# Performance work log

Measured on AMD Instinct MI355X. Metric: run time of the kernel, lower is better.

The kernel has to match this reference:

```python
import jax, jax.numpy as jnp
import numpy as np

# Static dims
N = 512        # nodes
T = 8          # window_size
E = 16384      # edges per timestep
F0, H1, FP = 128, 256, 64   # feat_proj_dims
FN = 16        # noise dim
WIN = FP + FN  # WLE in_channels = 80
WH = 128       # WLE hidden
D_SSM = 1      # TLSSM d_model = d_ssm = 1 (scalar per node pair)
D_STATE = 16
D_CONV = 4
CONV_DIM = D_SSM + 2 * D_STATE          # 33
D_IN = 2 * D_SSM + 2 * D_STATE + 1      # z, xBC, dt -> 35
PRED = 1


def setup_inputs() -> dict:
    key = jax.random.key(0)
    ks = jax.random.split(key, 24)
    s = 0.05
    rn = lambda k, shp: jax.random.normal(k, shp, dtype=jnp.float32) * s
    return {
        "edge_index": jax.random.randint(ks[0], (T, 2, E), 0, N, dtype=jnp.int64),
        "edge_weight": jax.random.uniform(ks[1], (T, E), dtype=jnp.float32),
        "feats": jax.random.normal(ks[2], (T, N, F0), dtype=jnp.float32),
        "noise": jax.random.normal(ks[3], (T, N, FN), dtype=jnp.float32),
        # feat_proj MLP
        "Wp1": rn(ks[4], (F0, H1)), "bp1": jnp.zeros((H1,), jnp.float32),
        "Wp2": rn(ks[5], (H1, FP)), "bp2": jnp.zeros((FP,), jnp.float32),
        # WeightedLinkEncoder
        "wle_W1": rn(ks[6], (WIN, WH)), "wle_b1": jnp.zeros((WH,), jnp.float32),
        "wle_W2": rn(ks[7], (WH, WH)), "wle_b2": jnp.zeros((WH,), jnp.float32),
        "wle_W3": rn(ks[8], (WH, WH)), "wle_b3": jnp.zeros((WH,), jnp.float32),
        "wle_w4": rn(ks[9], (WH, 1)), "wle_b4": jnp.zeros((1,), jnp.float32),
        # TLSSM (Mamba2-style stepwise)
        "W_in": rn(ks[10], (D_SSM, D_IN)),
        "conv_w": rn(ks[11], (CONV_DIM, D_CONV)),
        "conv_b": jnp.zeros((CONV_DIM,), jnp.float32),
        "dt_bias": jnp.zeros((1,), jnp.float32),
        "A_log": jnp.zeros((1,), jnp.float32),
        "D_skip": jnp.ones((1,), jnp.float32) * s,
        "W_out": rn(ks[12], (D_SSM, D_SSM)),
    }


def _forward(edge_index, edge_weight, feats, noise,
             Wp1, bp1, Wp2, bp2,
             wle_W1, wle_b1, wle_W2, wle_b2, wle_W3, wle_b3, wle_w4, wle_b4,
             W_in, conv_w, conv_b, dt_bias, A_log, D_skip, W_out):
    # feat_proj: stacked Linear+ReLU, vectorized over timesteps
    h = jax.nn.relu(feats @ Wp1 + bp1)
    h = jax.nn.relu(h @ Wp2 + bp2)              # [T, N, FP]
    emb = jnp.concatenate([h, noise], axis=-1)

    # WeightedLinkEncoder: node MLP -> weighted sparse propagation -> edge score
    def wle(x, ei, ew):
        hh = jax.nn.relu(x @ wle_W1 + wle_b1)                       # [N, WH]
        msg = ew[:, None] * hh[ei[1]]                               # gather neighbors
        agg = jax.ops.segment_sum(msg, ei[0], num_segments=N)      # scatter-add
        h2 = jax.nn.relu((hh + agg) @ wle_W2 + wle_b2)
        ef = h2[ei[0]] * h2[ei[1]]                                 # per-edge hadamard
        s = jax.nn.relu(ef @ wle_W3 + wle_b3) @ wle_w4 + wle_b4    # [E, 1]
        return s[:, 0]

    scores = jax.vmap(wle)(emb, edge_index, edge_weight)            # [T, E]

    # SparseTensor(...).to_dense(): densify edge scores to N x N per step
    def dens(ei, s):
        return jnp.zeros((N, N), scores.dtype).at[ei[0], ei[1]].set(s)

    dense = jax.vmap(dens)(edge_index, scores).reshape(T, N * N, D_SSM)

    # TLSSM stepwise recurrence over the window, batch = N*N
    A = -jnp.exp(A_log)  # [1]

    def step(carry, xt):
        conv_state, ssm_state = carry                    # [BN,CONV_DIM,D_CONV], [BN,D_SSM,D_STATE]
        zxbcdt = xt @ W_in                               # [BN, D_IN]
        z, xBC, dt = jnp.split(zxbcdt, [D_SSM, D_SSM + CONV_DIM], axis=-1)
        conv_state = jnp.concatenate([conv_state[:, :, 1:], xBC[:, :, None]], axis=-1)
        xBC = jax.nn.silu(jnp.sum(conv_state * conv_w, axis=-1) + conv_b)
        x_, Bm, Cm = jnp.split(xBC, [D_SSM, D_SSM + D_STATE], axis=-1)
        dt = jax.nn.softplus(dt + dt_bias)               # [BN, 1]
        dA = jnp.exp(dt * A)                             # [BN, 1]
        ssm_state = ssm_state * dA[:, :, None] + (dt * x_)[:, :, None] * Bm[:, None, :]
        y = jnp.sum(ssm_state * Cm[:, None, :], axis=-1) + D_skip * x_
        y = y * jax.nn.silu(z)
        return (conv_state, ssm_state), y @ W_out

    conv0 = jnp.zeros((N * N, CONV_DIM, D_CONV), jnp.float32)
    ssm0 = jnp.zeros((N * N, D_SSM, D_STATE), jnp.float32)
    _, ys = jax.lax.scan(step, (conv0, ssm0), dense)     # [T, BN, 1]
    out = ys.reshape(T, N, N)[-PRED:]                    # pred_flag=True: last pred_size steps
    return out


def reference(edge_index, edge_weight, feats, noise,
              Wp1, bp1, Wp2, bp2,
              wle_W1, wle_b1, wle_W2, wle_b2, wle_W3, wle_b3, wle_w4, wle_b4,
              W_in, conv_w, conv_b, dt_bias, A_log, D_skip, W_out):
    return _forward(edge_index, edge_weight, feats, noise,
                    Wp1, bp1, Wp2, bp2,
                    wle_W1, wle_b1, wle_W2, wle_b2, wle_W3, wle_b3, wle_w4, wle_b4,
                    W_in, conv_w, conv_b, dt_bias, A_log, D_skip, W_out)
```

## Files before the change

kernel.cpp:

```cpp
#include <hip/hip_runtime.h>
#include <math.h>

#define Nn 512
#define Tt 8
#define Ee 16384
#define NNc (Nn*Nn)
#define TNr (Tt*Nn)
#define TE  (Tt*Ee)
#define CAP 128

typedef __bf16 bf16x8 __attribute__((ext_vector_type(8)));
typedef float  f32x4  __attribute__((ext_vector_type(4)));
union BU { uint4 q; bf16x8 v; };

__device__ __forceinline__ void dec2(float x0, float x1, unsigned &hi, unsigned &lo){
    unsigned u0 = __float_as_uint(x0), u1 = __float_as_uint(x1);
    unsigned t0 = u0 + 0x7FFFu + ((u0>>16)&1u);
    unsigned t1 = u1 + 0x7FFFu + ((u1>>16)&1u);
    hi = (t0>>16) | (t1 & 0xFFFF0000u);
    float h0 = __uint_as_float(t0 & 0xFFFF0000u);
    float h1 = __uint_as_float(t1 & 0xFFFF0000u);
    float l0 = x0 - h0, l1 = x1 - h1;
    unsigned v0 = __float_as_uint(l0), v1 = __float_as_uint(l1);
    unsigned s0 = v0 + 0x7FFFu + ((v0>>16)&1u);
    unsigned s1 = v1 + 0x7FFFu + ((v1>>16)&1u);
    lo = (s0>>16) | (s1 & 0xFFFF0000u);
}

__global__ __launch_bounds__(256) void k_pf(
    const int* __restrict__ ei, const float* __restrict__ W3,
    unsigned short* __restrict__ w3h, unsigned short* __restrict__ w3l,
    int* __restrict__ cnt, int* __restrict__ tag, float4* __restrict__ out4,
    const float* __restrict__ feats, const float* __restrict__ noise,
    const float* __restrict__ Wp1, const float* __restrict__ bp1,
    const float* __restrict__ Wp2, const float* __restrict__ bp2,
    const float* __restrict__ W1, const float* __restrict__ b1,
    float* __restrict__ hh)
{
    __shared__ float sfeat[16][128];
    __shared__ float sh1[16][256];
    __shared__ float semb[16][80];
    int tid = threadIdx.x;
    if (blockIdx.x < 64){
        int e = blockIdx.x*256 + tid;
        int a = ei[7*2*Ee + e], b = ei[7*2*Ee + Ee + e];
        int cell = a*Nn + b;
#pragma unroll
        for (int t=0;t<8;++t) tag[t*NNc + cell] = 0;
        if (e < TNr) cnt[e] = 0;
        float4 z = {0.f,0.f,0.f,0.f};
#pragma unroll
        for (int q=0;q<4;++q) out4[q*16384 + e] = z;
        int i    = e & 7;
        int lane = (e>>3) & 63;
        int jt   = (e>>9) & 7;
        int kt   = e>>12;
        int k = kt*32 + (lane>>4)*8 + i;
        int j = jt*16 + (lane&15);
        float x = W3[k*128 + j];
        unsigned u = __float_as_uint(x);
        unsigned t = u + 0x7FFFu + ((u>>16)&1u);
        w3h[e] = (unsigned short)(t>>16);
        float hf = __uint_as_float(t & 0xFFFF0000u);
        float lf = x - hf;
        unsigned v = __float_as_uint(lf);
        unsigned s = v + 0x7FFFu + ((v>>16)&1u);
        w3l[e] = (unsigned short)(s>>16);
        return;
    }
    int r0 = (blockIdx.x - 64) * 16;
#pragma unroll
    for (int k = 0; k < 8; ++k) {
        int lin = k*256 + tid;
        sfeat[lin>>7][lin&127] = feats[(size_t)r0*128 + lin];
    }
    {
        int r = tid>>4, k = tid&15;
        semb[r][64+k] = noise[(size_t)(r0+r)*16 + k];
    }
    __syncthreads();
    {
        int j = tid;
        float acc[16];
#pragma unroll
        for (int r=0;r<16;++r) acc[r]=0.f;
        for (int i=0;i<128;i+=4) {
            float w0=Wp1[(i+0)*256+j], w1=Wp1[(i+1)*256+j];
            float w2=Wp1[(i+2)*256+j], w3=Wp1[(i+3)*256+j];
#pragma unroll
            for (int r=0;r<16;++r) {
                float4 f = *(const float4*)&sfeat[r][i];
                acc[r] += f.x*w0 + f.y*w1 + f.z*w2 + f.w*w3;
            }
        }
        float b = bp1[j];
#pragma unroll
        for (int r=0;r<16;++r) sh1[r][j] = fmaxf(acc[r]+b, 0.f);
    }
    __syncthreads();
    {
        int jo = tid & 63;
        int rr = tid >> 6;
        float b2v = bp2[jo];
        for (int rg=0; rg<4; ++rg) {
            int r = rg*4 + rr;
            float a2 = 0.f;
            for (int i=0;i<256;i+=4) {
                float4 f = *(const float4*)&sh1[r][i];
                a2 += f.x*Wp2[(i+0)*64+jo] + f.y*Wp2[(i+1)*64+jo]
                    + f.z*Wp2[(i+2)*64+jo] + f.w*Wp2[(i+3)*64+jo];
            }
            semb[r][jo] = fmaxf(a2+b2v, 0.f);
        }
    }
    __syncthreads();
    {
        int j = tid & 127;
        int rb = (tid>>7)*8;
        float acc[8];
#pragma unroll
        for (int r=0;r<8;++r) acc[r]=0.f;
        for (int i=0;i<80;i+=4) {
            float w0=W1[(i+0)*128+j], w1=W1[(i+1)*128+j];
            float w2=W1[(i+2)*128+j], w3=W1[(i+3)*128+j];
#pragma unroll
            for (int r=0;r<8;++r) {
                float4 f = *(const float4*)&semb[rb+r][i];
                acc[r] += f.x*w0 + f.y*w1 + f.z*w2 + f.w*w3;
            }
        }
        float b = b1[j];
#pragma unroll
        for (int r=0;r<8;++r) hh[(size_t)(r0+rb+r)*128 + j] = fmaxf(acc[r]+b, 0.f);
    }
}

__global__ __launch_bounds__(256) void k_histtag(
    const int* __restrict__ ei, const float* __restrict__ ew,
    int* __restrict__ cnt, int2* __restrict__ bucket2, int* __restrict__ tag)
{
    int g = blockIdx.x*256 + threadIdx.x;
    int t = g>>14, e = g&(Ee-1);
    int a = ei[t*2*Ee + e];
    int b = ei[t*2*Ee + Ee + e];
    int cell = t*Nn + a;
    int pos = atomicAdd(&cnt[cell], 1);
    if (pos < CAP) bucket2[(size_t)cell*CAP + pos] = make_int2(b, __float_as_int(ew[g]));
    atomicMax(&tag[t*NNc + a*Nn + b], g+1);
}

__global__ __launch_bounds__(256) void k_sw(
    const float* __restrict__ hh, const int* __restrict__ cnt,
    const int2* __restrict__ bucket2,
    const float* __restrict__ W2, const float* __restrict__ b2,
    float* __restrict__ h2)
{
    __shared__ float sx[2][128];
    int dloc = threadIdx.x >> 7;
    int ch = threadIdx.x & 127;
    int bidd = blockIdx.x*2 + dloc;
    int t = bidd >> 9;
    int n = cnt[bidd]; n = n < CAP ? n : CAP;
    const int2* __restrict__ bk = &bucket2[(size_t)bidd*CAP];
    const float* __restrict__ hht = &hh[(size_t)t*Nn*128];
    float acc = hh[(size_t)bidd*128 + ch];
    int i = 0;
    for (; i+1 < n; i += 2){
        int2 p0 = bk[i], p1 = bk[i+1];
        acc += __int_as_float(p0.y)*hht[(size_t)p0.x*128 + ch]
             + __int_as_float(p1.y)*hht[(size_t)p1.x*128 + ch];
    }
    if (i < n){
        int2 p = bk[i];
        acc += __int_as_float(p.y)*hht[(size_t)p.x*128 + ch];
    }
    sx[dloc][ch] = acc;
    __syncthreads();
    float s = 0.f;
    for (int i2=0; i2<128; i2+=4){
        float4 x = *(const float4*)&sx[dloc][i2];
        s += x.x*W2[(i2+0)*128+ch] + x.y*W2[(i2+1)*128+ch]
           + x.z*W2[(i2+2)*128+ch] + x.w*W2[(i2+3)*128+ch];
    }
    h2[(size_t)bidd*128 + ch] = fmaxf(s + b2[ch], 0.f);
}

__global__ __launch_bounds__(512) void k_edge9(
    const int* __restrict__ ei, const float* __restrict__ h2,
    const uint4* __restrict__ w3h, const uint4* __restrict__ w3l,
    const float* __restrict__ b3, const float* __restrict__ w4,
    const float* __restrict__ b4, float* __restrict__ sc)
{
    __shared__ uint4 sBh[2048];
    __shared__ uint4 sBl[2048];
    int tid = threadIdx.x;
    int bid = blockIdx.x;
#pragma unroll
    for (int q=0;q<4;++q){
        sBh[q*512+tid] = w3h[q*512+tid];
        sBl[q*512+tid] = w3l[q*512+tid];
    }
    int tb  = bid >> 6;
    int e0b = (bid & 63) * 256;
    int w   = tid >> 6, lane = tid & 63;
    int e0w = e0b + w*32;
    int r16 = lane & 15, g4 = lane >> 4;

    const int* __restrict__ eit = &ei[tb*2*Ee];
    int a0 = eit[e0w + r16],      s0 = eit[Ee + e0w + r16];
    int a1 = eit[e0w + 16 + r16], s1 = eit[Ee + e0w + 16 + r16];
    const float* __restrict__ pa0 = &h2[(size_t)(tb*Nn+a0)*128];
    const float* __restrict__ pb0 = &h2[(size_t)(tb*Nn+s0)*128];
    const float* __restrict__ pa1 = &h2[(size_t)(tb*Nn+a1)*128];
    const float* __restrict__ pb1 = &h2[(size_t)(tb*Nn+s1)*128];

    f32x4 acc0[8], acc1[8];
#pragma unroll
    for (int jt=0;jt<8;++jt){
        acc0[jt] = (f32x4){0.f,0.f,0.f,0.f};
        acc1[jt] = (f32x4){0.f,0.f,0.f,0.f};
    }

    float4 rA0,rA1,rB0,rB1,rC0,rC1,rD0,rD1;
#define LOADK(kt) { int k0=(kt)*32+g4*8; \
    rA0=*(const float4*)&pa0[k0]; rA1=*(const float4*)&pa0[k0+4]; \
    rB0=*(const float4*)&pb0[k0]; rB1=*(const float4*)&pb0[k0+4]; \
    rC0=*(const float4*)&pa1[k0]; rC1=*(const float4*)&pa1[k0+4]; \
    rD0=*(const float4*)&pb1[k0]; rD1=*(const float4*)&pb1[k0+4]; }

    BU ah0[2], al0[2], ah1[2], al1[2];
#define DECK(s) { uint4 hq,lq; \
    dec2(rA0.x*rB0.x, rA0.y*rB0.y, hq.x, lq.x); \
    dec2(rA0.z*rB0.z, rA0.w*rB0.w, hq.y, lq.y); \
    dec2(rA1.x*rB1.x, rA1.y*rB1.y, hq.z, lq.z); \
    dec2(rA1.z*rB1.z, rA1.w*rB1.w, hq.w, lq.w); \
    ah0[s].q=hq; al0[s].q=lq; \
    dec2(rC0.x*rD0.x, rC0.y*rD0.y, hq.x, lq.x); \
    dec2(rC0.z*rD0.z, rC0.w*rD0.w, hq.y, lq.y); \
    dec2(rC1.x*rD1.x, rC1.y*rD1.y, hq.z, lq.z); \
    dec2(rC1.z*rD1.z, rC1.w*rD1.w, hq.w, lq.w); \
    ah1[s].q=hq; al1[s].q=lq; }

    LOADK(0)
    DECK(0)
    __syncthreads();
#pragma unroll
    for (int kt=0;kt<4;++kt){
        if (kt < 3) LOADK(kt+1)
        const int s = kt & 1;
#pragma unroll
        for (int jt=0;jt<8;++jt){
            BU Bh, Bl;
            Bh.q = sBh[(kt*8+jt)*64 + lane];
            Bl.q = sBl[(kt*8+jt)*64 + lane];
            acc0[jt] = __builtin_amdgcn_mfma_f32_16x16x32_bf16(ah0[s].v, Bh.v, acc0[jt], 0,0,0);
            acc0[jt] = __builtin_amdgcn_mfma_f32_16x16x32_bf16(ah0[s].v, Bl.v, acc0[jt], 0,0,0);
            acc0[jt] = __builtin_amdgcn_mfma_f32_16x16x32_bf16(al0[s].v, Bh.v, acc0[jt], 0,0,0);
            acc1[jt] = __builtin_amdgcn_mfma_f32_16x16x32_bf16(ah1[s].v, Bh.v, acc1[jt], 0,0,0);
            acc1[jt] = __builtin_amdgcn_mfma_f32_16x16x32_bf16(ah1[s].v, Bl.v, acc1[jt], 0,0,0);
            acc1[jt] = __builtin_amdgcn_mfma_f32_16x16x32_bf16(al1[s].v, Bh.v, acc1[jt], 0,0,0);
        }
        if (kt < 3) DECK((kt+1)&1)
    }

    float b4v = b4[0];
    float b3v[8], w4v[8];
#pragma unroll
    for (int jt=0;jt<8;++jt){ b3v[jt] = b3[jt*16 + r16]; w4v[jt] = w4[jt*16 + r16]; }
#pragma unroll
    for (int r=0;r<4;++r){
        float p0 = 0.f, p1 = 0.f;
#pragma unroll
        for (int jt=0;jt<8;++jt){
            p0 += fmaxf(acc0[jt][r] + b3v[jt], 0.f) * w4v[jt];
            p1 += fmaxf(acc1[jt][r] + b3v[jt], 0.f) * w4v[jt];
        }
        p0 += __shfl_xor(p0,1); p0 += __shfl_xor(p0,2);
        p0 += __shfl_xor(p0,4); p0 += __shfl_xor(p0,8);
        p1 += __shfl_xor(p1,1); p1 += __shfl_xor(p1,2);
        p1 += __shfl_xor(p1,4); p1 += __shfl_xor(p1,8);
        if (r16 == 0){
            sc[(size_t)tb*Ee + e0w + g4*4 + r]      = p0 + b4v;
            sc[(size_t)tb*Ee + e0w + 16 + g4*4 + r] = p1 + b4v;
        }
    }
}

__global__ __launch_bounds__(256) void k_ssm2(
    const int* __restrict__ ei, const int* __restrict__ tag,
    const float* __restrict__ sc,
    const float* __restrict__ W_in, const float* __restrict__ conv_w,
    const float* __restrict__ conv_b, const float* __restrict__ dt_bias,
    const float* __restrict__ A_log, const float* __restrict__ D_skip,
    const float* __restrict__ W_out, float* __restrict__ out)
{
    __shared__ float scw[132], scb[33], swin[35];
    int tid = threadIdx.x;
    if (tid < 132) scw[tid] = conv_w[tid];
    if (tid < 33)  scb[tid] = conv_b[tid];
    if (tid < 35)  swin[tid] = W_in[tid];
    __syncthreads();

    int e = blockIdx.x*256 + tid;
    int a = ei[7*2*Ee + e], b = ei[7*2*Ee + Ee + e];
    int cell = a*Nn + b;
    float x[8];
#pragma unroll
    for (int t=0;t<8;++t){
        int tg = tag[t*NNc + cell];
        x[t] = (tg > 0) ? sc[tg-1] : 0.f;
    }

    float A    = -expf(A_log[0]);
    float dtb  = dt_bias[0];
    float dsk  = D_skip[0];
    float wout = W_out[0];
    float win_z = swin[0], win_dt = swin[34];

    float ssm[16];
#pragma unroll
    for (int q=0;q<16;++q) ssm[q]=0.f;
    float h0=0.f,h1=0.f,h2v=0.f;
    float y=0.f;
    for (int t=0;t<8;++t){
        float xt = x[t];
        float act[33];
#pragma unroll
        for (int c=0;c<33;++c){
            float s = h0*scw[c*4+0] + h1*scw[c*4+1] + h2v*scw[c*4+2] + xt*scw[c*4+3];
            float pre = swin[1+c]*s + scb[c];
            act[c] = pre / (1.f + expf(-pre));
        }
        float x_ = act[0];
        float dtr = xt*win_dt + dtb;
        float dt  = (dtr > 20.f) ? dtr : log1pf(expf(dtr));
        float dA  = expf(dt*A);
        float dx  = dt*x_;
        float yv = 0.f;
#pragma unroll
        for (int q=0;q<16;++q){
            ssm[q] = ssm[q]*dA + dx*act[1+q];
            yv += ssm[q]*act[17+q];
        }
        yv += dsk*x_;
        float z = xt*win_z;
        yv *= z / (1.f + expf(-z));
        y = yv;
        h0=h1; h1=h2v; h2v=xt;
    }
    out[cell] = y*wout;
}

extern "C" void kernel_launch(void* const* d_in, const int* in_sizes, int n_in,
                              void* d_out, int out_size, void* d_ws, size_t ws_size,
                              hipStream_t stream)
{
    const int*   ei    = (const int*)d_in[0];
    const float* ew    = (const float*)d_in[1];
    const float* feats = (const float*)d_in[2];
    const float* noise = (const float*)d_in[3];
    const float* Wp1=(const float*)d_in[4];  const float* bp1=(const float*)d_in[5];
    const float* Wp2=(const float*)d_in[6];  const float* bp2=(const float*)d_in[7];
    const float* W1 =(const float*)d_in[8];  const float* b1 =(const float*)d_in[9];
    const float* W2 =(const float*)d_in[10]; const float* b2 =(const float*)d_in[11];
    const float* W3 =(const float*)d_in[12]; const float* b3 =(const float*)d_in[13];
    const float* w4 =(const float*)d_in[14]; const float* b4 =(const float*)d_in[15];
    const float* W_in  =(const float*)d_in[16]; const float* conv_w=(const float*)d_in[17];
    const float* conv_b=(const float*)d_in[18]; const float* dt_bias=(const float*)d_in[19];
    const float* A_log =(const float*)d_in[20]; const float* D_skip=(const float*)d_in[21];
    const float* W_out =(const float*)d_in[22];

    float* out = (float*)d_out;
    float* ws  = (float*)d_ws;
    float* hh    = ws;
    float* h2    = hh    + 524288;
    float* sc    = h2    + 524288;
    int*   cnt   = (int*)(sc + 131072);
    int*   tag   = cnt + TNr;
    int2*  bucket2 = (int2*)(tag + 2097152);
    unsigned short* w3h = (unsigned short*)(bucket2 + (size_t)TNr*CAP);
    unsigned short* w3l = w3h + 16384;

    k_pf      <<<320, 256, 0, stream>>>(ei, W3, w3h, w3l, cnt, tag, (float4*)out,
                                        feats, noise, Wp1, bp1, Wp2, bp2, W1, b1, hh);
    k_histtag <<<TE/256, 256, 0, stream>>>(ei, ew, cnt, bucket2, tag);
    k_sw      <<<TNr/2, 256, 0, stream>>>(hh, cnt, bucket2, W2, b2, h2);
    k_edge9   <<<512, 512, 0, stream>>>(ei, h2, (const uint4*)w3h, (const uint4*)w3l,
                                        b3, w4, b4, sc);
    k_ssm2    <<<Ee/256, 256, 0, stream>>>(ei, tag, sc, W_in, conv_w, conv_b,
                                           dt_bias, A_log, D_skip, W_out, out);
}
```

Before: 107.2 us.

## Make feature-projection MLP wave-private to replace block barriers with wave barriers

The per-row feature projection MLP (two Linear+ReLU layers plus the first link-encoder layer) is reorganised so each 64-lane wave owns four rows end to end. That lets the block-wide __syncthreads be replaced by wave barriers. Weight loads are widened to float4/float2 so each lane computes several output columns. The likely cost is that Wp1, Wp2 and W1 are now fetched once per wave rather than once per block, raising global/L2 weight traffic. Register use per lane also changes.

```diff
diff --git a/kernel.cpp b/kernel.cpp
--- a/kernel.cpp
+++ b/kernel.cpp
@@ -68,70 +68,96 @@
         w3l[e] = (unsigned short)(s>>16);
         return;
     }
-    int r0 = (blockIdx.x - 64) * 16;
-#pragma unroll
-    for (int k = 0; k < 8; ++k) {
-        int lin = k*256 + tid;
-        sfeat[lin>>7][lin&127] = feats[(size_t)r0*128 + lin];
-    }
+    int w = tid >> 6, lane = tid & 63;
+    int lr = w*4;
+    int r0 = (blockIdx.x - 64)*16 + lr;
     {
-        int r = tid>>4, k = tid&15;
-        semb[r][64+k] = noise[(size_t)(r0+r)*16 + k];
-    }
-    __syncthreads();
+        const float4* __restrict__ src = (const float4*)&feats[(size_t)r0*128];
+        float4 v0 = src[lane], v1 = src[64+lane];
+        ((float4*)&sfeat[lr][0])[lane]    = v0;
+        ((float4*)&sfeat[lr][0])[64+lane] = v1;
+    }
     {
-        int j = tid;
-        float acc[16];
-#pragma unroll
-        for (int r=0;r<16;++r) acc[r]=0.f;
-        for (int i=0;i<128;i+=4) {
-            float w0=Wp1[(i+0)*256+j], w1=Wp1[(i+1)*256+j];
-            float w2=Wp1[(i+2)*256+j], w3=Wp1[(i+3)*256+j];
-#pragma unroll
-            for (int r=0;r<16;++r) {
-                float4 f = *(const float4*)&sfeat[r][i];
-                acc[r] += f.x*w0 + f.y*w1 + f.z*w2 + f.w*w3;
+        int r = lane >> 4, k = lane & 15;
+        semb[lr+r][64+k] = noise[(size_t)(r0+r)*16 + k];
+    }
+    __builtin_amdgcn_wave_barrier();
+    {
+        int jb = lane*4;
+        float acc[4][4];
+#pragma unroll
+        for (int r=0;r<4;++r)
+#pragma unroll
+            for (int q=0;q<4;++q) acc[r][q]=0.f;
+        for (int i=0;i<128;i+=4){
+            float4 w0 = *(const float4*)&Wp1[(i+0)*256 + jb];
+            float4 w1 = *(const float4*)&Wp1[(i+1)*256 + jb];
+            float4 w2 = *(const float4*)&Wp1[(i+2)*256 + jb];
+            float4 w3 = *(const float4*)&Wp1[(i+3)*256 + jb];
+#pragma unroll
+            for (int r=0;r<4;++r){
+                float4 f = *(const float4*)&sfeat[lr+r][i];
+                acc[r][0] += f.x*w0.x + f.y*w1.x + f.z*w2.x + f.w*w3.x;
+                acc[r][1] += f.x*w0.y + f.y*w1.y + f.z*w2.y + f.w*w3.y;
+                acc[r][2] += f.x*w0.z + f.y*w1.z + f.z*w2.z + f.w*w3.z;
+                acc[r][3] += f.x*w0.w + f.y*w1.w + f.z*w2.w + f.w*w3.w;
             }
         }
-        float b = bp1[j];
-#pragma unroll
-        for (int r=0;r<16;++r) sh1[r][j] = fmaxf(acc[r]+b, 0.f);
-    }
-    __syncthreads();
+        float4 b = *(const float4*)&bp1[jb];
+#pragma unroll
+        for (int r=0;r<4;++r){
+            float4 o;
+            o.x = fmaxf(acc[r][0]+b.x, 0.f);
+            o.y = fmaxf(acc[r][1]+b.y, 0.f);
+            o.z = fmaxf(acc[r][2]+b.z, 0.f);
+            o.w = fmaxf(acc[r][3]+b.w, 0.f);
+            *(float4*)&sh1[lr+r][jb] = o;
+        }
+    }
+    __builtin_amdgcn_wave_barrier();
     {
-        int jo = tid & 63;
-        int rr = tid >> 6;
-        float b2v = bp2[jo];
-        for (int rg=0; rg<4; ++rg) {
-            int r = rg*4 + rr;
-            float a2 = 0.f;
-            for (int i=0;i<256;i+=4) {
-                float4 f = *(const float4*)&sh1[r][i];
-                a2 += f.x*Wp2[(i+0)*64+jo] + f.y*Wp2[(i+1)*64+jo]
-                    + f.z*Wp2[(i+2)*64+jo] + f.w*Wp2[(i+3)*64+jo];
+        float a2[4] = {0.f,0.f,0.f,0.f};
+        for (int i=0;i<256;i+=4){
+            float w0 = Wp2[(i+0)*64 + lane];
+            float w1 = Wp2[(i+1)*64 + lane];
+            float w2 = Wp2[(i+2)*64 + lane];
+            float w3 = Wp2[(i+3)*64 + lane];
+#pragma unroll
+            for (int r=0;r<4;++r){
+                float4 f = *(const float4*)&sh1[lr+r][i];
+                a2[r] += f.x*w0 + f.y*w1 + f.z*w2 + f.w*w3;
             }
-            semb[r][jo] = fmaxf(a2+b2v, 0.f);
-        }
-    }
-    __syncthreads();
+        }
+        float b = bp2[lane];
+#pragma unroll
+        for (int r=0;r<4;++r) semb[lr+r][lane] = fmaxf(a2[r]+b, 0.f);
+    }
+    __builtin_amdgcn_wave_barrier();
     {
-        int j = tid & 127;
-        int rb = (tid>>7)*8;
-        float acc[8];
-#pragma unroll
-        for (int r=0;r<8;++r) acc[r]=0.f;
-        for (int i=0;i<80;i+=4) {
-            float w0=W1[(i+0)*128+j], w1=W1[(i+1)*128+j];
-            float w2=W1[(i+2)*128+j], w3=W1[(i+3)*128+j];
-#pragma unroll
-            for (int r=0;r<8;++r) {
-                float4 f = *(const float4*)&semb[rb+r][i];
-                acc[r] += f.x*w0 + f.y*w1 + f.z*w2 + f.w*w3;
+        int j2 = lane*2;
+        float a3[4][2];
+#pragma unroll
+        for (int r=0;r<4;++r){ a3[r][0]=0.f; a3[r][1]=0.f; }
+        for (int i=0;i<80;i+=4){
+            float2 w0 = *(const float2*)&W1[(i+0)*128 + j2];
+            float2 w1 = *(const float2*)&W1[(i+1)*128 + j2];
+            float2 w2 = *(const float2*)&W1[(i+2)*128 + j2];
+            float2 w3 = *(const float2*)&W1[(i+3)*128 + j2];
+#pragma unroll
+            for (int r=0;r<4;++r){
+                float4 f = *(const float4*)&semb[lr+r][i];
+                a3[r][0] += f.x*w0.x + f.y*w1.x + f.z*w2.x + f.w*w3.x;
+                a3[r][1] += f.x*w0.y + f.y*w1.y + f.z*w2.y + f.w*w3.y;
             }
         }
-        float b = b1[j];
-#pragma unroll
-        for (int r=0;r<8;++r) hh[(size_t)(r0+rb+r)*128 + j] = fmaxf(acc[r]+b, 0.f);
+        float2 bb = *(const float2*)&b1[j2];
+#pragma unroll
+        for (int r=0;r<4;++r){
+            float2 o;
+            o.x = fmaxf(a3[r][0]+bb.x, 0.f);
+            o.y = fmaxf(a3[r][1]+bb.y, 0.f);
+            *(float2*)&hh[(size_t)(r0+r)*128 + j2] = o;
+        }
     }
 }
 
```

Result: slower. 111.4 us (+3.9%).

## Move feature-projection MLP to split-bf16 MFMA and fuse it with edge histogram

Applied to the files above, without the earlier changes.

The three dense layers (feat_proj two layers plus the first WLE layer) move from scalar FP32 FMA loops to MFMA 16x16x32 bf16. A three-product hi/lo split keeps accuracy close to FP32. A new prep kernel pre-splits and swizzles Wp1, Wp2 and W1 into bf16 hi/lo tiles. The MLP blocks and the edge histogram/tag atomics now run in one launch, removing a kernel boundary and letting the two workloads overlap. The cost is an extra weight-conversion pass on every call and more scratch space, and the reduced-precision split may change the output slightly.

```diff
diff --git a/kernel.cpp b/kernel.cpp
--- a/kernel.cpp
+++ b/kernel.cpp
@@ -27,22 +27,38 @@
     lo = (s0>>16) | (s1 & 0xFFFF0000u);
 }
 
-__global__ __launch_bounds__(256) void k_pf(
+__device__ __forceinline__ void splitw(float x, unsigned short* ph, unsigned short* pl, int idx){
+    unsigned u = __float_as_uint(x);
+    unsigned t = u + 0x7FFFu + ((u>>16)&1u);
+    ph[idx] = (unsigned short)(t>>16);
+    float hf = __uint_as_float(t & 0xFFFF0000u);
+    float lf = x - hf;
+    unsigned v = __float_as_uint(lf);
+    unsigned s = v + 0x7FFFu + ((v>>16)&1u);
+    pl[idx] = (unsigned short)(s>>16);
+}
+
+#define DECA(Ah, Al, xa, ya) { uint4 hq, lq; \
+    dec2(xa.x, xa.y, hq.x, lq.x); \
+    dec2(xa.z, xa.w, hq.y, lq.y); \
+    dec2(ya.x, ya.y, hq.z, lq.z); \
+    dec2(ya.z, ya.w, hq.w, lq.w); \
+    Ah.q = hq; Al.q = lq; }
+
+__global__ __launch_bounds__(256) void k_prep(
     const int* __restrict__ ei, const float* __restrict__ W3,
+    const float* __restrict__ Wp1, const float* __restrict__ Wp2,
+    const float* __restrict__ W1,
     unsigned short* __restrict__ w3h, unsigned short* __restrict__ w3l,
-    int* __restrict__ cnt, int* __restrict__ tag, float4* __restrict__ out4,
-    const float* __restrict__ feats, const float* __restrict__ noise,
-    const float* __restrict__ Wp1, const float* __restrict__ bp1,
-    const float* __restrict__ Wp2, const float* __restrict__ bp2,
-    const float* __restrict__ W1, const float* __restrict__ b1,
-    float* __restrict__ hh)
-{
-    __shared__ float sfeat[16][128];
-    __shared__ float sh1[16][256];
-    __shared__ float semb[16][80];
+    unsigned short* __restrict__ p1h, unsigned short* __restrict__ p1l,
+    unsigned short* __restrict__ p2h, unsigned short* __restrict__ p2l,
+    unsigned short* __restrict__ p3h, unsigned short* __restrict__ p3l,
+    int* __restrict__ cnt, int* __restrict__ tag, float4* __restrict__ out4)
+{
     int tid = threadIdx.x;
-    if (blockIdx.x < 64){
-        int e = blockIdx.x*256 + tid;
+    int bid = blockIdx.x;
+    if (bid < 64){
+        int e = bid*256 + tid;
         int a = ei[7*2*Ee + e], b = ei[7*2*Ee + Ee + e];
         int cell = a*Nn + b;
 #pragma unroll
@@ -55,98 +71,165 @@
         int lane = (e>>3) & 63;
         int jt   = (e>>9) & 7;
         int kt   = e>>12;
-        int k = kt*32 + (lane>>4)*8 + i;
-        int j = jt*16 + (lane&15);
-        float x = W3[k*128 + j];
-        unsigned u = __float_as_uint(x);
-        unsigned t = u + 0x7FFFu + ((u>>16)&1u);
-        w3h[e] = (unsigned short)(t>>16);
-        float hf = __uint_as_float(t & 0xFFFF0000u);
-        float lf = x - hf;
-        unsigned v = __float_as_uint(lf);
-        unsigned s = v + 0x7FFFu + ((v>>16)&1u);
-        w3l[e] = (unsigned short)(s>>16);
+        splitw(W3[(kt*32+(lane>>4)*8+i)*128 + jt*16+(lane&15)], w3h, w3l, e);
         return;
     }
-    int r0 = (blockIdx.x - 64) * 16;
-#pragma unroll
-    for (int k = 0; k < 8; ++k) {
-        int lin = k*256 + tid;
-        sfeat[lin>>7][lin&127] = feats[(size_t)r0*128 + lin];
+    if (bid < 192){
+        int idx = (bid-64)*256 + tid;
+        int i=idx&7, lane=(idx>>3)&63, jt=(idx>>9)&15, kt=idx>>13;
+        splitw(Wp1[(kt*32+(lane>>4)*8+i)*256 + jt*16+(lane&15)], p1h, p1l, idx);
+        return;
+    }
+    if (bid < 256){
+        int idx = (bid-192)*256 + tid;
+        int i=idx&7, lane=(idx>>3)&63, jt=(idx>>9)&3, kt=idx>>11;
+        splitw(Wp2[(kt*32+(lane>>4)*8+i)*64 + jt*16+(lane&15)], p2h, p2l, idx);
+        return;
     }
     {
-        int r = tid>>4, k = tid&15;
-        semb[r][64+k] = noise[(size_t)(r0+r)*16 + k];
+        int idx = (bid-256)*256 + tid;
+        int i=idx&7, lane=(idx>>3)&63, jt=(idx>>9)&7, kt=idx>>12;
+        int k = kt*32+(lane>>4)*8+i;
+        float v = (k < 80) ? W1[k*128 + jt*16+(lane&15)] : 0.f;
+        splitw(v, p3h, p3l, idx);
+    }
+}
+
+__global__ __launch_bounds__(256) void k_mid(
+    const int* __restrict__ ei, const float* __restrict__ ew,
+    int* __restrict__ cnt, int2* __restrict__ bucket2, int* __restrict__ tag,
+    const float* __restrict__ feats, const float* __restrict__ noise,
+    const uint4* __restrict__ p1h, const uint4* __restrict__ p1l,
+    const float* __restrict__ bp1,
+    const uint4* __restrict__ p2h, const uint4* __restrict__ p2l,
+    const float* __restrict__ bp2,
+    const uint4* __restrict__ p3h, const uint4* __restrict__ p3l,
+    const float* __restrict__ b1, float* __restrict__ hh)
+{
+    __shared__ float h1s[32][260];
+    __shared__ float embs[32][100];
+    int tid = threadIdx.x;
+    if (blockIdx.x >= 128){
+        int g = (blockIdx.x - 128)*256 + tid;
+        int t = g>>14, e = g&(Ee-1);
+        int a = ei[t*2*Ee + e];
+        int b = ei[t*2*Ee + Ee + e];
+        int cell = t*Nn + a;
+        int pos = atomicAdd(&cnt[cell], 1);
+        if (pos < CAP) bucket2[(size_t)cell*CAP + pos] = make_int2(b, __float_as_int(ew[g]));
+        atomicMax(&tag[t*NNc + a*Nn + b], g+1);
+        return;
+    }
+    int w = tid >> 6, lane = tid & 63;
+    int r16 = lane & 15, g4 = lane >> 4;
+    int r0 = blockIdx.x*32;
+    {
+        int row = tid >> 3, c2 = (tid & 7)*2;
+        float2 nz = *(const float2*)&noise[(size_t)(r0+row)*16 + c2];
+        embs[row][64+c2] = nz.x; embs[row][64+c2+1] = nz.y;
+        embs[row][80+c2] = 0.f;  embs[row][80+c2+1] = 0.f;
+    }
+    const float* __restrict__ pa0 = &feats[(size_t)(r0 + r16)*128];
+    const float* __restrict__ pa1 = &feats[(size_t)(r0 + 16 + r16)*128];
+    {
+        f32x4 a1[4][2];
+#pragma unroll
+        for (int jl=0;jl<4;++jl){ a1[jl][0]=(f32x4){0,0,0,0}; a1[jl][1]=(f32x4){0,0,0,0}; }
+#pragma unroll
+        for (int kt=0;kt<4;++kt){
+            int k0 = kt*32 + g4*8;
+            BU Ah0, Al0, Ah1, Al1;
+            { float4 xa=*(const float4*)&pa0[k0], ya=*(const float4*)&pa0[k0+4]; DECA(Ah0,Al0,xa,ya) }
+            { float4 xa=*(const float4*)&pa1[k0], ya=*(const float4*)&pa1[k0+4]; DECA(Ah1,Al1,xa,ya) }
+#pragma unroll
+            for (int jl=0;jl<4;++jl){
+                int jt = w*4 + jl;
+                BU Bh, Bl;
+                Bh.q = p1h[(kt*16+jt)*64 + lane];
+                Bl.q = p1l[(kt*16+jt)*64 + lane];
+                a1[jl][0] = __builtin_amdgcn_mfma_f32_16x16x32_bf16(Ah0.v, Bh.v, a1[jl][0], 0,0,0);
+                a1[jl][0] = __builtin_amdgcn_mfma_f32_16x16x32_bf16(Ah0.v, Bl.v, a1[jl][0], 0,0,0);
+                a1[jl][0] = __builtin_amdgcn_mfma_f32_16x16x32_bf16(Al0.v, Bh.v, a1[jl][0], 0,0,0);
+                a1[jl][1] = __builtin_amdgcn_mfma_f32_16x16x32_bf16(Ah1.v, Bh.v, a1[jl][1], 0,0,0);
+                a1[jl][1] = __builtin_amdgcn_mfma_f32_16x16x32_bf16(Ah1.v, Bl.v, a1[jl][1], 0,0,0);
+                a1[jl][1] = __builtin_amdgcn_mfma_f32_16x16x32_bf16(Al1.v, Bh.v, a1[jl][1], 0,0,0);
+            }
+        }
+#pragma unroll
+        for (int jl=0;jl<4;++jl){
+            int jcol = (w*4+jl)*16 + r16;
+            float b = bp1[jcol];
+#pragma unroll
+            for (int r=0;r<4;++r){
+                h1s[g4*4+r][jcol]      = fmaxf(a1[jl][0][r] + b, 0.f);
+                h1s[16+g4*4+r][jcol]   = fmaxf(a1[jl][1][r] + b, 0.f);
+            }
+        }
     }
     __syncthreads();
     {
-        int j = tid;
-        float acc[16];
-#pragma unroll
-        for (int r=0;r<16;++r) acc[r]=0.f;
-        for (int i=0;i<128;i+=4) {
-            float w0=Wp1[(i+0)*256+j], w1=Wp1[(i+1)*256+j];
-            float w2=Wp1[(i+2)*256+j], w3=Wp1[(i+3)*256+j];
-#pragma unroll
-            for (int r=0;r<16;++r) {
-                float4 f = *(const float4*)&sfeat[r][i];
-                acc[r] += f.x*w0 + f.y*w1 + f.z*w2 + f.w*w3;
-            }
-        }
-        float b = bp1[j];
-#pragma unroll
-        for (int r=0;r<16;++r) sh1[r][j] = fmaxf(acc[r]+b, 0.f);
+        f32x4 a2[2];
+        a2[0]=(f32x4){0,0,0,0}; a2[1]=(f32x4){0,0,0,0};
+#pragma unroll
+        for (int kt=0;kt<8;++kt){
+            int k0 = kt*32 + g4*8;
+            BU Ah0, Al0, Ah1, Al1;
+            { float4 xa=*(const float4*)&h1s[r16][k0],    ya=*(const float4*)&h1s[r16][k0+4];    DECA(Ah0,Al0,xa,ya) }
+            { float4 xa=*(const float4*)&h1s[16+r16][k0], ya=*(const float4*)&h1s[16+r16][k0+4]; DECA(Ah1,Al1,xa,ya) }
+            BU Bh, Bl;
+            Bh.q = p2h[(kt*4+w)*64 + lane];
+            Bl.q = p2l[(kt*4+w)*64 + lane];
+            a2[0] = __builtin_amdgcn_mfma_f32_16x16x32_bf16(Ah0.v, Bh.v, a2[0], 0,0,0);
+            a2[0] = __builtin_amdgcn_mfma_f32_16x16x32_bf16(Ah0.v, Bl.v, a2[0], 0,0,0);
+            a2[0] = __builtin_amdgcn_mfma_f32_16x16x32_bf16(Al0.v, Bh.v, a2[0], 0,0,0);
+            a2[1] = __builtin_amdgcn_mfma_f32_16x16x32_bf16(Ah1.v, Bh.v, a2[1], 0,0,0);
+            a2[1] = __builtin_amdgcn_mfma_f32_16x16x32_bf16(Ah1.v, Bl.v, a2[1], 0,0,0);
+            a2[1] = __builtin_amdgcn_mfma_f32_16x16x32_bf16(Al1.v, Bh.v, a2[1], 0,0,0);
+        }
+        int jcol = w*16 + r16;
+        float b = bp2[jcol];
+#pragma unroll
+        for (int r=0;r<4;++r){
+            embs[g4*4+r][jcol]    = fmaxf(a2[0][r] + b, 0.f);
+            embs[16+g4*4+r][jcol] = fmaxf(a2[1][r] + b, 0.f);
+        }
     }
     __syncthreads();
     {
-        int jo = tid & 63;
-        int rr = tid >> 6;
-        float b2v = bp2[jo];
-        for (int rg=0; rg<4; ++rg) {
-            int r = rg*4 + rr;
-            float a2 = 0.f;
-            for (int i=0;i<256;i+=4) {
-                float4 f = *(const float4*)&sh1[r][i];
-                a2 += f.x*Wp2[(i+0)*64+jo] + f.y*Wp2[(i+1)*64+jo]
-                    + f.z*Wp2[(i+2)*64+jo] + f.w*Wp2[(i+3)*64+jo];
+        f32x4 a3[2][2];
+#pragma unroll
+        for (int jl=0;jl<2;++jl){ a3[jl][0]=(f32x4){0,0,0,0}; a3[jl][1]=(f32x4){0,0,0,0}; }
+#pragma unroll
+        for (int kt=0;kt<3;++kt){
+            int k0 = kt*32 + g4*8;
+            BU Ah0, Al0, Ah1, Al1;
+            { float4 xa=*(const float4*)&embs[r16][k0],    ya=*(const float4*)&embs[r16][k0+4];    DECA(Ah0,Al0,xa,ya) }
+            { float4 xa=*(const float4*)&embs[16+r16][k0], ya=*(const float4*)&embs[16+r16][k0+4]; DECA(Ah1,Al1,xa,ya) }
+#pragma unroll
+            for (int jl=0;jl<2;++jl){
+                int jt = w*2 + jl;
+                BU Bh, Bl;
+                Bh.q = p3h[(kt*8+jt)*64 + lane];
+                Bl.q = p3l[(kt*8+jt)*64 + lane];
+                a3[jl][0] = __builtin_amdgcn_mfma_f32_16x16x32_bf16(Ah0.v, Bh.v, a3[jl][0], 0,0,0);
+                a3[jl][0] = __builtin_amdgcn_mfma_f32_16x16x32_bf16(Ah0.v, Bl.v, a3[jl][0], 0,0,0);
+                a3[jl][0] = __builtin_amdgcn_mfma_f32_16x16x32_bf16(Al0.v, Bh.v, a3[jl][0], 0,0,0);
+                a3[jl][1] = __builtin_amdgcn_mfma_f32_16x16x32_bf16(Ah1.v, Bh.v, a3[jl][1], 0,0,0);
+                a3[jl][1] = __builtin_amdgcn_mfma_f32_16x16x32_bf16(Ah1.v, Bl.v, a3[jl][1], 0,0,0);
+                a3[jl][1] = __builtin_amdgcn_mfma_f32_16x16x32_bf16(Al1.v, Bh.v, a3[jl][1], 0,0,0);
             }
-            semb[r][jo] = fmaxf(a2+b2v, 0.f);
-        }
-    }
-    __syncthreads();
-    {
-        int j = tid & 127;
-        int rb = (tid>>7)*8;
-        float acc[8];
-#pragma unroll
-        for (int r=0;r<8;++r) acc[r]=0.f;
-        for (int i=0;i<80;i+=4) {
-            float w0=W1[(i+0)*128+j], w1=W1[(i+1)*128+j];
-            float w2=W1[(i+2)*128+j], w3=W1[(i+3)*128+j];
-#pragma unroll
-            for (int r=0;r<8;++r) {
-                float4 f = *(const float4*)&semb[rb+r][i];
-                acc[r] += f.x*w0 + f.y*w1 + f.z*w2 + f.w*w3;
+        }
+#pragma unroll
+        for (int jl=0;jl<2;++jl){
+            int jcol = (w*2+jl)*16 + r16;
+            float b = b1[jcol];
+#pragma unroll
+            for (int r=0;r<4;++r){
+                hh[(size_t)(r0+g4*4+r)*128 + jcol]    = fmaxf(a3[jl][0][r] + b, 0.f);
+                hh[(size_t)(r0+16+g4*4+r)*128 + jcol] = fmaxf(a3[jl][1][r] + b, 0.f);
             }
         }
-        float b = b1[j];
-#pragma unroll
-        for (int r=0;r<8;++r) hh[(size_t)(r0+rb+r)*128 + j] = fmaxf(acc[r]+b, 0.f);
-    }
-}
-
-__global__ __launch_bounds__(256) void k_histtag(
-    const int* __restrict__ ei, const float* __restrict__ ew,
-    int* __restrict__ cnt, int2* __restrict__ bucket2, int* __restrict__ tag)
-{
-    int g = blockIdx.x*256 + threadIdx.x;
-    int t = g>>14, e = g&(Ee-1);
-    int a = ei[t*2*Ee + e];
-    int b = ei[t*2*Ee + Ee + e];
-    int cell = t*Nn + a;
-    int pos = atomicAdd(&cnt[cell], 1);
-    if (pos < CAP) bucket2[(size_t)cell*CAP + pos] = make_int2(b, __float_as_int(ew[g]));
-    atomicMax(&tag[t*NNc + a*Nn + b], g+1);
+    }
 }
 
 __global__ __launch_bounds__(256) void k_sw(
@@ -380,13 +463,23 @@
     int2*  bucket2 = (int2*)(tag + 2097152);
     unsigned short* w3h = (unsigned short*)(bucket2 + (size_t)TNr*CAP);
     unsigned short* w3l = w3h + 16384;
-
-    k_pf      <<<320, 256, 0, stream>>>(ei, W3, w3h, w3l, cnt, tag, (float4*)out,
-                                        feats, noise, Wp1, bp1, Wp2, bp2, W1, b1, hh);
-    k_histtag <<<TE/256, 256, 0, stream>>>(ei, ew, cnt, bucket2, tag);
-    k_sw      <<<TNr/2, 256, 0, stream>>>(hh, cnt, bucket2, W2, b2, h2);
-    k_edge9   <<<512, 512, 0, stream>>>(ei, h2, (const uint4*)w3h, (const uint4*)w3l,
-                                        b3, w4, b4, sc);
-    k_ssm2    <<<Ee/256, 256, 0, stream>>>(ei, tag, sc, W_in, conv_w, conv_b,
-                                           dt_bias, A_log, D_skip, W_out, out);
-}
+    unsigned short* p1h = w3l + 16384;
+    unsigned short* p1l = p1h + 32768;
+    unsigned short* p2h = p1l + 32768;
+    unsigned short* p2l = p2h + 16384;
+    unsigned short* p3h = p2l + 16384;
+    unsigned short* p3l = p3h + 12288;
+
+    k_prep <<<304, 256, 0, stream>>>(ei, W3, Wp1, Wp2, W1,
+                                     w3h, w3l, p1h, p1l, p2h, p2l, p3h, p3l,
+                                     cnt, tag, (float4*)out);
+    k_mid  <<<640, 256, 0, stream>>>(ei, ew, cnt, bucket2, tag, feats, noise,
+                                     (const uint4*)p1h, (const uint4*)p1l, bp1,
+                                     (const uint4*)p2h, (const uint4*)p2l, bp2,
+                                     (const uint4*)p3h, (const uint4*)p3l, b1, hh);
+    k_sw   <<<TNr/2, 256, 0, stream>>>(hh, cnt, bucket2, W2, b2, h2);
+    k_edge9<<<512, 512, 0, stream>>>(ei, h2, (const uint4*)w3h, (const uint4*)w3l,
+                                     b3, w4, b4, sc);
+    k_ssm2 <<<Ee/256, 256, 0, stream>>>(ei, tag, sc, W_in, conv_w, conv_b,
+                                        dt_bias, A_log, D_skip, W_out, out);
+}
```

New measurement: 95.58 us. 1.12x faster.
